# Kernel tuning notes

Measured on AMD Instinct MI355X. Metric: run time of the kernel, lower is better.

Reference implementation:

```python
import jax, jax.numpy as jnp
import numpy as np

D_MODEL = 1024
N_HEADS = 16
HEAD_DIM = D_MODEL // N_HEADS


def setup_inputs() -> dict:
    key = jax.random.key(0)
    k1, k2, k3 = jax.random.split(key, 3)
    x = jax.random.normal(k1, (8, 1024, D_MODEL), dtype=jnp.float32)
    qkv_w = jax.random.normal(k2, (3 * D_MODEL, D_MODEL), dtype=jnp.float32) * 0.02
    qkv_b = jnp.zeros((3 * D_MODEL,), dtype=jnp.float32)
    proj_w = jax.random.normal(k3, (D_MODEL, D_MODEL), dtype=jnp.float32) * 0.02
    proj_b = jnp.zeros((D_MODEL,), dtype=jnp.float32)
    return {"x": x, "qkv_w": qkv_w, "qkv_b": qkv_b, "proj_w": proj_w, "proj_b": proj_b}


def reference(x, qkv_w, qkv_b, proj_w, proj_b):
    B, N, C = x.shape
    H, Dh = N_HEADS, HEAD_DIM
    # fused QKV projection (torch Linear: x @ W^T + b)
    qkv = x @ qkv_w.T + qkv_b                      # [B, N, 3C]
    qkv = qkv.reshape(B, N, 3, H, Dh).transpose(2, 0, 3, 1, 4)  # [3, B, H, N, Dh]
    q, k, v = qkv[0], qkv[1], qkv[2]
    scale = Dh ** -0.5
    attn = jnp.einsum("bhnd,bhmd->bhnm", q, k) * scale  # [B, H, N, N]
    attn = jax.nn.softmax(attn, axis=-1)
    out = jnp.einsum("bhnm,bhmd->bhnd", attn, v)        # [B, H, N, Dh]
    out = out.transpose(0, 2, 1, 3).reshape(B, N, C)
    return out @ proj_w.T + proj_b
```

## Files before the change

kernel.cpp:

```cpp
#include <hip/hip_runtime.h>
#include <hip/hip_bf16.h>
#include <stdint.h>

#define D_MODEL 1024
#define NHEADS  16
#define HDIM    64
#define SEQ     1024
#define BATCH   8

typedef __bf16 bf16;
typedef bf16  bf16x8 __attribute__((ext_vector_type(8)));
typedef float f32x4  __attribute__((ext_vector_type(4)));
typedef uint32_t u32;

__device__ __forceinline__ int swzi(int row, int col) {
    return (row << 6) + (col ^ ((row & 7) << 3));
}

__device__ __forceinline__ void gload_lds16(const bf16* g, bf16* l) {
    __builtin_amdgcn_global_load_lds(
        (const __attribute__((address_space(1))) void*)g,
        (__attribute__((address_space(3))) void*)l, 16, 0, 0);
}

__global__ void cvt_kernel(const float* __restrict__ in, bf16* __restrict__ out, int n) {
    int i = (blockIdx.x * 256 + threadIdx.x) * 8;
    if (i >= n) return;
    float4 a = *reinterpret_cast<const float4*>(in + i);
    float4 b = *reinterpret_cast<const float4*>(in + i + 4);
    union { bf16 h[8]; uint4 u; } pk;
    pk.h[0] = (bf16)a.x; pk.h[1] = (bf16)a.y; pk.h[2] = (bf16)a.z; pk.h[3] = (bf16)a.w;
    pk.h[4] = (bf16)b.x; pk.h[5] = (bf16)b.y; pk.h[6] = (bf16)b.z; pk.h[7] = (bf16)b.w;
    *reinterpret_cast<uint4*>(out + i) = pk.u;
}

__device__ __forceinline__ void gemm_tile_acc(
    const bf16* __restrict__ A, const bf16* __restrict__ B, int K,
    int m0, int n0, bf16* As, bf16* Bs,
    f32x4 acc[4][4], int wr, int wc, int lane, int tid)
{
    for (int kt = 0; kt < K; kt += 64) {
        __syncthreads();
#pragma unroll
        for (int c = 0; c < 4; ++c) {
            int chunk = tid + c * 256;
            int r   = chunk >> 3;
            int j   = chunk & 7;
            int jg  = j ^ (r & 7);
            gload_lds16(A + (size_t)(m0 + r) * K + kt + jg * 8, As + chunk * 8);
            gload_lds16(B + (size_t)(n0 + r) * K + kt + jg * 8, Bs + chunk * 8);
        }
        __syncthreads();
#pragma unroll
        for (int kk = 0; kk < 2; ++kk) {
            bf16x8 af[4], bfr[4];
#pragma unroll
            for (int t = 0; t < 4; ++t) {
                af[t]  = *reinterpret_cast<const bf16x8*>(As + swzi(wr * 64 + t * 16 + (lane & 15), kk * 32 + ((lane >> 4) << 3)));
                bfr[t] = *reinterpret_cast<const bf16x8*>(Bs + swzi(wc * 64 + t * 16 + (lane & 15), kk * 32 + ((lane >> 4) << 3)));
            }
#pragma unroll
            for (int i = 0; i < 4; ++i)
#pragma unroll
                for (int j2 = 0; j2 < 4; ++j2)
                    acc[i][j2] = __builtin_amdgcn_mfma_f32_16x16x32_bf16(af[i], bfr[j2], acc[i][j2], 0, 0, 0);
        }
    }
}

__global__ __launch_bounds__(256)
void qkv_gemm(const bf16* __restrict__ X, const bf16* __restrict__ W,
              const float* __restrict__ bias,
              bf16* __restrict__ q_ws, bf16* __restrict__ k_ws, bf16* __restrict__ vt_ws)
{
    __shared__ __align__(16) bf16 As[128 * 64];
    __shared__ __align__(16) bf16 Bs[128 * 64];
    const int NB = 3072 / 128;
    int bm = blockIdx.x / NB, bn = blockIdx.x % NB;
    int m0 = bm * 128, n0 = bn * 128;
    int tid = threadIdx.x, lane = tid & 63, w = tid >> 6;
    int wr = w >> 1, wc = w & 1;
    f32x4 acc[4][4];
#pragma unroll
    for (int i = 0; i < 4; ++i)
#pragma unroll
        for (int j = 0; j < 4; ++j) acc[i][j] = (f32x4){0.f, 0.f, 0.f, 0.f};

    gemm_tile_acc(X, W, 1024, m0, n0, As, Bs, acc, wr, wc, lane, tid);

#pragma unroll
    for (int i = 0; i < 4; ++i) {
        int mbase = m0 + wr * 64 + i * 16 + ((lane >> 4) << 2);
#pragma unroll
        for (int j = 0; j < 4; ++j) {
            int col = n0 + wc * 64 + j * 16 + (lane & 15);
            int which = col >> 10, rem = col & 1023;
            int h = rem >> 6, d = rem & 63;
            float bi = bias[col];
            int b = mbase >> 10, nrow0 = mbase & 1023;
            int bh = b * NHEADS + h;
            if (which == 2) {
                union { bf16 h4[4]; uint2 u; } vp;
#pragma unroll
                for (int r = 0; r < 4; ++r) vp.h4[r] = (bf16)(acc[i][j][r] + bi);
                *reinterpret_cast<uint2*>(vt_ws + ((size_t)bh * HDIM + d) * SEQ + nrow0) = vp.u;
            } else {
                bf16* dst = (which == 0) ? q_ws : k_ws;
                float scl = (which == 0) ? 0.125f : 1.0f;
#pragma unroll
                for (int r = 0; r < 4; ++r) {
                    float v = (acc[i][j][r] + bi) * scl;
                    dst[((size_t)bh * SEQ + nrow0 + r) * HDIM + d] = (bf16)v;
                }
            }
        }
    }
}

__global__ __launch_bounds__(256)
void proj_gemm(const bf16* __restrict__ Ao, const bf16* __restrict__ W,
               const float* __restrict__ bias, float* __restrict__ out)
{
    __shared__ __align__(16) bf16 As[128 * 64];
    __shared__ __align__(16) bf16 Bs[128 * 64];
    const int NB = 1024 / 128;
    int bm = blockIdx.x / NB, bn = blockIdx.x % NB;
    int m0 = bm * 128, n0 = bn * 128;
    int tid = threadIdx.x, lane = tid & 63, w = tid >> 6;
    int wr = w >> 1, wc = w & 1;
    f32x4 acc[4][4];
#pragma unroll
    for (int i = 0; i < 4; ++i)
#pragma unroll
        for (int j = 0; j < 4; ++j) acc[i][j] = (f32x4){0.f, 0.f, 0.f, 0.f};

    gemm_tile_acc(Ao, W, 1024, m0, n0, As, Bs, acc, wr, wc, lane, tid);

#pragma unroll
    for (int i = 0; i < 4; ++i) {
        int mbase = m0 + wr * 64 + i * 16 + ((lane >> 4) << 2);
#pragma unroll
        for (int j = 0; j < 4; ++j) {
            int col = n0 + wc * 64 + j * 16 + (lane & 15);
            float bi = bias[col];
#pragma unroll
            for (int r = 0; r < 4; ++r)
                out[(size_t)(mbase + r) * D_MODEL + col] = acc[i][j][r] + bi;
        }
    }
}

__global__ __launch_bounds__(256)
void attn_kernel(const bf16* __restrict__ Q, const bf16* __restrict__ K,
                 const bf16* __restrict__ Vt, bf16* __restrict__ AO)
{
    __shared__ __align__(16) bf16 kl[64 * 64];
    __shared__ __align__(16) bf16 vl[64 * 64];
    int bh = blockIdx.x & 127;
    int qt = blockIdx.x >> 7;
    int tid = threadIdx.x, lane = tid & 63, w = tid >> 6;
    int g = lane >> 4, q = lane & 15;
    const bf16* Qb  = Q  + (size_t)bh * SEQ * HDIM;
    const bf16* Kb  = K  + (size_t)bh * SEQ * HDIM;
    const bf16* Vtb = Vt + (size_t)bh * HDIM * SEQ;

    int qrow = qt * 64 + w * 16 + q;
    bf16x8 qf[2];
#pragma unroll
    for (int kk = 0; kk < 2; ++kk)
        qf[kk] = *reinterpret_cast<const bf16x8*>(Qb + (size_t)qrow * HDIM + kk * 32 + (g << 3));

    f32x4 o[4];
#pragma unroll
    for (int dt = 0; dt < 4; ++dt) o[dt] = (f32x4){0.f, 0.f, 0.f, 0.f};
    float mrun = -1e30f, lrun = 0.f;

    int srcA = ((g & 1) << 5) + q;
    int srcB = srcA + 16;
    bool hi = (g >> 1) != 0;

    for (int t = 0; t < 16; ++t) {
        __syncthreads();
#pragma unroll
        for (int c = 0; c < 2; ++c) {
            int chunk = tid + c * 256;
            int r  = chunk >> 3;
            int j  = chunk & 7;
            int jg = j ^ (r & 7);
            gload_lds16(Kb  + (size_t)(t * 64 + r) * HDIM + jg * 8, kl + chunk * 8);
            gload_lds16(Vtb + (size_t)r * SEQ + t * 64 + jg * 8,    vl + chunk * 8);
        }
        __syncthreads();

        f32x4 s[4];
#pragma unroll
        for (int nt = 0; nt < 4; ++nt) {
            s[nt] = (f32x4){0.f, 0.f, 0.f, 0.f};
#pragma unroll
            for (int kk = 0; kk < 2; ++kk) {
                bf16x8 kf = *reinterpret_cast<const bf16x8*>(
                    kl + swzi(nt * 16 + q, kk * 32 + (g << 3)));
                s[nt] = __builtin_amdgcn_mfma_f32_16x16x32_bf16(kf, qf[kk], s[nt], 0, 0, 0);
            }
        }

        float pm = s[0][0];
#pragma unroll
        for (int nt = 0; nt < 4; ++nt)
#pragma unroll
            for (int r = 0; r < 4; ++r) pm = fmaxf(pm, s[nt][r]);
        pm = fmaxf(pm, __shfl_xor(pm, 16));
        pm = fmaxf(pm, __shfl_xor(pm, 32));
        float mnew  = fmaxf(mrun, pm);
        float alpha = __expf(mrun - mnew);

        u32 pk[4][2];
        float psum = 0.f;
#pragma unroll
        for (int nt = 0; nt < 4; ++nt)
#pragma unroll
            for (int half = 0; half < 2; ++half) {
                float pa = __expf(s[nt][2 * half]     - mnew);
                float pb = __expf(s[nt][2 * half + 1] - mnew);
                psum += pa + pb;
                union { bf16 h[2]; u32 u; } pw;
                pw.h[0] = (bf16)pa; pw.h[1] = (bf16)pb;
                pk[nt][half] = pw.u;
            }
        psum += __shfl_xor(psum, 16);
        psum += __shfl_xor(psum, 32);
        lrun = lrun * alpha + psum;
        mrun = mnew;
#pragma unroll
        for (int dt = 0; dt < 4; ++dt) o[dt] *= alpha;

#pragma unroll
        for (int ks = 0; ks < 2; ++ks) {
            union { u32 u[4]; bf16x8 v; } pb;
            u32 a0 = __shfl((int)pk[2 * ks][0],     srcA);
            u32 a1 = __shfl((int)pk[2 * ks + 1][0], srcA);
            pb.u[0] = hi ? a1 : a0;
            u32 b0 = __shfl((int)pk[2 * ks][1],     srcA);
            u32 b1 = __shfl((int)pk[2 * ks + 1][1], srcA);
            pb.u[1] = hi ? b1 : b0;
            u32 c0 = __shfl((int)pk[2 * ks][0],     srcB);
            u32 c1 = __shfl((int)pk[2 * ks + 1][0], srcB);
            pb.u[2] = hi ? c1 : c0;
            u32 d0 = __shfl((int)pk[2 * ks][1],     srcB);
            u32 d1 = __shfl((int)pk[2 * ks + 1][1], srcB);
            pb.u[3] = hi ? d1 : d0;
#pragma unroll
            for (int dt = 0; dt < 4; ++dt) {
                bf16x8 vfr = *reinterpret_cast<const bf16x8*>(
                    vl + swzi(dt * 16 + q, ks * 32 + (g << 3)));
                o[dt] = __builtin_amdgcn_mfma_f32_16x16x32_bf16(vfr, pb.v, o[dt], 0, 0, 0);
            }
        }
    }

    int b = bh >> 4, h = bh & 15;
    float inv = 1.f / lrun;
    size_t base = ((size_t)b * SEQ + qrow) * D_MODEL + h * HDIM;
#pragma unroll
    for (int dt = 0; dt < 4; ++dt) {
        union { bf16 h4[4]; uint2 u; } ob;
#pragma unroll
        for (int r = 0; r < 4; ++r) ob.h4[r] = (bf16)(o[dt][r] * inv);
        *reinterpret_cast<uint2*>(AO + base + dt * 16 + (g << 2)) = ob.u;
    }
}

extern "C" void kernel_launch(void* const* d_in, const int* in_sizes, int n_in,
                              void* d_out, int out_size, void* d_ws, size_t ws_size,
                              hipStream_t stream) {
    const float* x      = (const float*)d_in[0];
    const float* qkv_w  = (const float*)d_in[1];
    const float* qkv_b  = (const float*)d_in[2];
    const float* proj_w = (const float*)d_in[3];
    const float* proj_b = (const float*)d_in[4];
    float* out = (float*)d_out;
    char* ws = (char*)d_ws;

    bf16* x_bf    = (bf16*)(ws);
    bf16* wqkv_bf = (bf16*)(ws + (size_t)(16 << 20));
    bf16* wproj_bf= (bf16*)(ws + (size_t)(22 << 20));
    bf16* q_ws    = (bf16*)(ws + (size_t)(24 << 20));
    bf16* k_ws    = (bf16*)(ws + (size_t)(40 << 20));
    bf16* vt_ws   = (bf16*)(ws + (size_t)(56 << 20));
    bf16* ao_ws   = x_bf;

    cvt_kernel<<<(8192 * 1024) / 2048, 256, 0, stream>>>(x, x_bf, 8192 * 1024);
    cvt_kernel<<<(3072 * 1024) / 2048, 256, 0, stream>>>(qkv_w, wqkv_bf, 3072 * 1024);
    cvt_kernel<<<(1024 * 1024) / 2048, 256, 0, stream>>>(proj_w, wproj_bf, 1024 * 1024);

    qkv_gemm<<<64 * 24, 256, 0, stream>>>(x_bf, wqkv_bf, qkv_b, q_ws, k_ws, vt_ws);
    attn_kernel<<<128 * 16, 256, 0, stream>>>(q_ws, k_ws, vt_ws, ao_ws);
    proj_gemm<<<64 * 8, 256, 0, stream>>>(ao_ws, wproj_bf, proj_b, out);
}
```

Before: 188.6 us.

## Process two query tiles per warp in attention, reusing K/V fragments, with exp2 lazy rescaling

Each attention block now covers 128 query rows instead of 64, with each warp handling two 16-row query groups. K and V fragments are loaded from LDS once per tile and reused for both groups, which halves the K/V global and LDS traffic per query. The softmax scale now folds in log2(e) so exp2f can replace expf. A lazy rescale skips the max update while the new max stays within 6 of the running one. The grid is halved, which cuts occupancy and wave count, and the larger fragment arrays raise register pressure.

```diff
diff --git a/kernel.cpp b/kernel.cpp
--- a/kernel.cpp
+++ b/kernel.cpp
@@ -106,7 +106,7 @@
                 *reinterpret_cast<uint2*>(vt_ws + ((size_t)bh * HDIM + d) * SEQ + nrow0) = vp.u;
             } else {
                 bf16* dst = (which == 0) ? q_ws : k_ws;
-                float scl = (which == 0) ? 0.125f : 1.0f;
+                float scl = (which == 0) ? 0.18033688011112042f : 1.0f;
 #pragma unroll
                 for (int r = 0; r < 4; ++r) {
                     float v = (acc[i][j][r] + bi) * scl;
@@ -164,109 +164,148 @@
     const bf16* Kb  = K  + (size_t)bh * SEQ * HDIM;
     const bf16* Vtb = Vt + (size_t)bh * HDIM * SEQ;
 
-    int qrow = qt * 64 + w * 16 + q;
-    bf16x8 qf[2];
-#pragma unroll
-    for (int kk = 0; kk < 2; ++kk)
-        qf[kk] = *reinterpret_cast<const bf16x8*>(Qb + (size_t)qrow * HDIM + kk * 32 + (g << 3));
-
-    f32x4 o[4];
-#pragma unroll
-    for (int dt = 0; dt < 4; ++dt) o[dt] = (f32x4){0.f, 0.f, 0.f, 0.f};
-    float mrun = -1e30f, lrun = 0.f;
+    int qrow0 = qt * 128 + w * 32;
+    bf16x8 qf[2][2];
+#pragma unroll
+    for (int qh = 0; qh < 2; ++qh)
+#pragma unroll
+        for (int kk = 0; kk < 2; ++kk)
+            qf[qh][kk] = *reinterpret_cast<const bf16x8*>(
+                Qb + (size_t)(qrow0 + qh * 16 + q) * HDIM + kk * 32 + (g << 3));
+
+    f32x4 o[2][4];
+#pragma unroll
+    for (int qh = 0; qh < 2; ++qh)
+#pragma unroll
+        for (int dt = 0; dt < 4; ++dt) o[qh][dt] = (f32x4){0.f, 0.f, 0.f, 0.f};
+    float mrun[2] = {-1e30f, -1e30f}, lrun[2] = {0.f, 0.f};
 
     int srcA = ((g & 1) << 5) + q;
     int srcB = srcA + 16;
     bool hi = (g >> 1) != 0;
 
+    const bf16* ksrc[2]; const bf16* vsrc[2]; bf16* kdst[2]; bf16* vdst[2];
+#pragma unroll
+    for (int c = 0; c < 2; ++c) {
+        int chunk = tid + c * 256;
+        int r  = chunk >> 3;
+        int j  = chunk & 7;
+        int jg = j ^ (r & 7);
+        ksrc[c] = Kb  + (size_t)r * HDIM + jg * 8;
+        vsrc[c] = Vtb + (size_t)r * SEQ + jg * 8;
+        kdst[c] = kl + chunk * 8;
+        vdst[c] = vl + chunk * 8;
+    }
+
     for (int t = 0; t < 16; ++t) {
         __syncthreads();
 #pragma unroll
         for (int c = 0; c < 2; ++c) {
-            int chunk = tid + c * 256;
-            int r  = chunk >> 3;
-            int j  = chunk & 7;
-            int jg = j ^ (r & 7);
-            gload_lds16(Kb  + (size_t)(t * 64 + r) * HDIM + jg * 8, kl + chunk * 8);
-            gload_lds16(Vtb + (size_t)r * SEQ + t * 64 + jg * 8,    vl + chunk * 8);
+            gload_lds16(ksrc[c], kdst[c]);
+            gload_lds16(vsrc[c], vdst[c]);
+            ksrc[c] += 64 * HDIM;
+            vsrc[c] += 64;
         }
         __syncthreads();
 
-        f32x4 s[4];
-#pragma unroll
-        for (int nt = 0; nt < 4; ++nt) {
-            s[nt] = (f32x4){0.f, 0.f, 0.f, 0.f};
-#pragma unroll
-            for (int kk = 0; kk < 2; ++kk) {
-                bf16x8 kf = *reinterpret_cast<const bf16x8*>(
+        bf16x8 kf[4][2];
+#pragma unroll
+        for (int nt = 0; nt < 4; ++nt)
+#pragma unroll
+            for (int kk = 0; kk < 2; ++kk)
+                kf[nt][kk] = *reinterpret_cast<const bf16x8*>(
                     kl + swzi(nt * 16 + q, kk * 32 + (g << 3)));
-                s[nt] = __builtin_amdgcn_mfma_f32_16x16x32_bf16(kf, qf[kk], s[nt], 0, 0, 0);
-            }
-        }
-
-        float pm = s[0][0];
-#pragma unroll
-        for (int nt = 0; nt < 4; ++nt)
-#pragma unroll
-            for (int r = 0; r < 4; ++r) pm = fmaxf(pm, s[nt][r]);
-        pm = fmaxf(pm, __shfl_xor(pm, 16));
-        pm = fmaxf(pm, __shfl_xor(pm, 32));
-        float mnew  = fmaxf(mrun, pm);
-        float alpha = __expf(mrun - mnew);
-
-        u32 pk[4][2];
-        float psum = 0.f;
-#pragma unroll
-        for (int nt = 0; nt < 4; ++nt)
-#pragma unroll
-            for (int half = 0; half < 2; ++half) {
-                float pa = __expf(s[nt][2 * half]     - mnew);
-                float pb = __expf(s[nt][2 * half + 1] - mnew);
-                psum += pa + pb;
-                union { bf16 h[2]; u32 u; } pw;
-                pw.h[0] = (bf16)pa; pw.h[1] = (bf16)pb;
-                pk[nt][half] = pw.u;
-            }
-        psum += __shfl_xor(psum, 16);
-        psum += __shfl_xor(psum, 32);
-        lrun = lrun * alpha + psum;
-        mrun = mnew;
-#pragma unroll
-        for (int dt = 0; dt < 4; ++dt) o[dt] *= alpha;
-
-#pragma unroll
-        for (int ks = 0; ks < 2; ++ks) {
-            union { u32 u[4]; bf16x8 v; } pb;
-            u32 a0 = __shfl((int)pk[2 * ks][0],     srcA);
-            u32 a1 = __shfl((int)pk[2 * ks + 1][0], srcA);
-            pb.u[0] = hi ? a1 : a0;
-            u32 b0 = __shfl((int)pk[2 * ks][1],     srcA);
-            u32 b1 = __shfl((int)pk[2 * ks + 1][1], srcA);
-            pb.u[1] = hi ? b1 : b0;
-            u32 c0 = __shfl((int)pk[2 * ks][0],     srcB);
-            u32 c1 = __shfl((int)pk[2 * ks + 1][0], srcB);
-            pb.u[2] = hi ? c1 : c0;
-            u32 d0 = __shfl((int)pk[2 * ks][1],     srcB);
-            u32 d1 = __shfl((int)pk[2 * ks + 1][1], srcB);
-            pb.u[3] = hi ? d1 : d0;
-#pragma unroll
-            for (int dt = 0; dt < 4; ++dt) {
-                bf16x8 vfr = *reinterpret_cast<const bf16x8*>(
+
+        u32 pkk[2][4][2];
+#pragma unroll
+        for (int qh = 0; qh < 2; ++qh) {
+            f32x4 s[4];
+#pragma unroll
+            for (int nt = 0; nt < 4; ++nt) {
+                s[nt] = (f32x4){0.f, 0.f, 0.f, 0.f};
+#pragma unroll
+                for (int kk = 0; kk < 2; ++kk)
+                    s[nt] = __builtin_amdgcn_mfma_f32_16x16x32_bf16(kf[nt][kk], qf[qh][kk], s[nt], 0, 0, 0);
+            }
+
+            float pm = fmaxf(fmaxf(s[0][0], s[0][1]), fmaxf(s[0][2], s[0][3]));
+            pm = fmaxf(fmaxf(pm, s[1][0]), fmaxf(s[1][1], s[1][2]));
+            pm = fmaxf(fmaxf(pm, s[1][3]), fmaxf(s[2][0], s[2][1]));
+            pm = fmaxf(fmaxf(pm, s[2][2]), fmaxf(s[2][3], s[3][0]));
+            pm = fmaxf(fmaxf(pm, s[3][1]), fmaxf(s[3][2], s[3][3]));
+            pm = fmaxf(pm, __shfl_xor(pm, 16));
+            pm = fmaxf(pm, __shfl_xor(pm, 32));
+
+            if (!__all(pm - mrun[qh] <= 6.f)) {
+                float mnew  = fmaxf(mrun[qh], pm);
+                float alpha = exp2f(mrun[qh] - mnew);
+                lrun[qh] *= alpha;
+                mrun[qh] = mnew;
+#pragma unroll
+                for (int dt = 0; dt < 4; ++dt) o[qh][dt] *= alpha;
+            }
+
+            float m2 = mrun[qh];
+            float psum = 0.f;
+#pragma unroll
+            for (int nt = 0; nt < 4; ++nt)
+#pragma unroll
+                for (int half = 0; half < 2; ++half) {
+                    float pa = exp2f(s[nt][2 * half]     - m2);
+                    float pb = exp2f(s[nt][2 * half + 1] - m2);
+                    psum += pa + pb;
+                    union { bf16 h[2]; u32 u; } pw;
+                    pw.h[0] = (bf16)pa; pw.h[1] = (bf16)pb;
+                    pkk[qh][nt][half] = pw.u;
+                }
+            psum += __shfl_xor(psum, 16);
+            psum += __shfl_xor(psum, 32);
+            lrun[qh] += psum;
+        }
+
+        bf16x8 vfr[4][2];
+#pragma unroll
+        for (int dt = 0; dt < 4; ++dt)
+#pragma unroll
+            for (int ks = 0; ks < 2; ++ks)
+                vfr[dt][ks] = *reinterpret_cast<const bf16x8*>(
                     vl + swzi(dt * 16 + q, ks * 32 + (g << 3)));
-                o[dt] = __builtin_amdgcn_mfma_f32_16x16x32_bf16(vfr, pb.v, o[dt], 0, 0, 0);
-            }
-        }
+
+#pragma unroll
+        for (int qh = 0; qh < 2; ++qh)
+#pragma unroll
+            for (int ks = 0; ks < 2; ++ks) {
+                union { u32 u[4]; bf16x8 v; } pb;
+                u32 a0 = __shfl((int)pkk[qh][2 * ks][0],     srcA);
+                u32 a1 = __shfl((int)pkk[qh][2 * ks + 1][0], srcA);
+                pb.u[0] = hi ? a1 : a0;
+                u32 b0 = __shfl((int)pkk[qh][2 * ks][1],     srcA);
+                u32 b1 = __shfl((int)pkk[qh][2 * ks + 1][1], srcA);
+                pb.u[1] = hi ? b1 : b0;
+                u32 c0 = __shfl((int)pkk[qh][2 * ks][0],     srcB);
+                u32 c1 = __shfl((int)pkk[qh][2 * ks + 1][0], srcB);
+                pb.u[2] = hi ? c1 : c0;
+                u32 d0 = __shfl((int)pkk[qh][2 * ks][1],     srcB);
+                u32 d1 = __shfl((int)pkk[qh][2 * ks + 1][1], srcB);
+                pb.u[3] = hi ? d1 : d0;
+#pragma unroll
+                for (int dt = 0; dt < 4; ++dt)
+                    o[qh][dt] = __builtin_amdgcn_mfma_f32_16x16x32_bf16(vfr[dt][ks], pb.v, o[qh][dt], 0, 0, 0);
+            }
     }
 
     int b = bh >> 4, h = bh & 15;
-    float inv = 1.f / lrun;
-    size_t base = ((size_t)b * SEQ + qrow) * D_MODEL + h * HDIM;
-#pragma unroll
-    for (int dt = 0; dt < 4; ++dt) {
-        union { bf16 h4[4]; uint2 u; } ob;
-#pragma unroll
-        for (int r = 0; r < 4; ++r) ob.h4[r] = (bf16)(o[dt][r] * inv);
-        *reinterpret_cast<uint2*>(AO + base + dt * 16 + (g << 2)) = ob.u;
+#pragma unroll
+    for (int qh = 0; qh < 2; ++qh) {
+        float inv = 1.f / lrun[qh];
+        size_t base = ((size_t)b * SEQ + qrow0 + qh * 16 + q) * D_MODEL + h * HDIM;
+#pragma unroll
+        for (int dt = 0; dt < 4; ++dt) {
+            union { bf16 h4[4]; uint2 u; } ob;
+#pragma unroll
+            for (int r = 0; r < 4; ++r) ob.h4[r] = (bf16)(o[qh][dt][r] * inv);
+            *reinterpret_cast<uint2*>(AO + base + dt * 16 + (g << 2)) = ob.u;
+        }
     }
 }
 
@@ -294,6 +333,6 @@
     cvt_kernel<<<(1024 * 1024) / 2048, 256, 0, stream>>>(proj_w, wproj_bf, 1024 * 1024);
 
     qkv_gemm<<<64 * 24, 256, 0, stream>>>(x_bf, wqkv_bf, qkv_b, q_ws, k_ws, vt_ws);
-    attn_kernel<<<128 * 16, 256, 0, stream>>>(q_ws, k_ws, vt_ws, ao_ws);
+    attn_kernel<<<128 * 8, 256, 0, stream>>>(q_ws, k_ws, vt_ws, ao_ws);
     proj_gemm<<<64 * 8, 256, 0, stream>>>(ao_ws, wproj_bf, proj_b, out);
 }
```

Measured after the change: 201.6 us. 6.9% more time.

## Use exp2 softmax with lazy rescaling, hoisted load addresses, and MFMA priority hints

Applied to the files above, without the earlier changes.

Folds log2(e) into the Q scale so the softmax can use exp2 directly. Rescaling of the output accumulator is skipped unless the running max grows by more than a threshold anywhere in the wave. Global-to-LDS source and destination pointers are precomputed once and advanced each iteration, and s_setprio is raised around the MFMA blocks. The lazy rescale leaves exponentials bounded by 2^6 in fp32/bf16 accumulation, which trades a small numerical risk for fewer multiplies per tile.

```diff
diff --git a/kernel.cpp b/kernel.cpp
--- a/kernel.cpp
+++ b/kernel.cpp
@@ -106,7 +106,7 @@
                 *reinterpret_cast<uint2*>(vt_ws + ((size_t)bh * HDIM + d) * SEQ + nrow0) = vp.u;
             } else {
                 bf16* dst = (which == 0) ? q_ws : k_ws;
-                float scl = (which == 0) ? 0.125f : 1.0f;
+                float scl = (which == 0) ? 0.18033688011112042f : 1.0f;
 #pragma unroll
                 for (int r = 0; r < 4; ++r) {
                     float v = (acc[i][j][r] + bi) * scl;
@@ -179,20 +179,32 @@
     int srcB = srcA + 16;
     bool hi = (g >> 1) != 0;
 
+    const bf16* ksrc[2]; const bf16* vsrc[2]; bf16* kdst[2]; bf16* vdst[2];
+#pragma unroll
+    for (int c = 0; c < 2; ++c) {
+        int chunk = tid + c * 256;
+        int r  = chunk >> 3;
+        int j  = chunk & 7;
+        int jg = j ^ (r & 7);
+        ksrc[c] = Kb  + (size_t)r * HDIM + jg * 8;
+        vsrc[c] = Vtb + (size_t)r * SEQ + jg * 8;
+        kdst[c] = kl + chunk * 8;
+        vdst[c] = vl + chunk * 8;
+    }
+
     for (int t = 0; t < 16; ++t) {
         __syncthreads();
 #pragma unroll
         for (int c = 0; c < 2; ++c) {
-            int chunk = tid + c * 256;
-            int r  = chunk >> 3;
-            int j  = chunk & 7;
-            int jg = j ^ (r & 7);
-            gload_lds16(Kb  + (size_t)(t * 64 + r) * HDIM + jg * 8, kl + chunk * 8);
-            gload_lds16(Vtb + (size_t)r * SEQ + t * 64 + jg * 8,    vl + chunk * 8);
+            gload_lds16(ksrc[c], kdst[c]);
+            gload_lds16(vsrc[c], vdst[c]);
+            ksrc[c] += 64 * HDIM;
+            vsrc[c] += 64;
         }
         __syncthreads();
 
         f32x4 s[4];
+        __builtin_amdgcn_s_setprio(1);
 #pragma unroll
         for (int nt = 0; nt < 4; ++nt) {
             s[nt] = (f32x4){0.f, 0.f, 0.f, 0.f};
@@ -203,58 +215,66 @@
                 s[nt] = __builtin_amdgcn_mfma_f32_16x16x32_bf16(kf, qf[kk], s[nt], 0, 0, 0);
             }
         }
-
-        float pm = s[0][0];
-#pragma unroll
-        for (int nt = 0; nt < 4; ++nt)
-#pragma unroll
-            for (int r = 0; r < 4; ++r) pm = fmaxf(pm, s[nt][r]);
+        __builtin_amdgcn_s_setprio(0);
+
+        float pm = fmaxf(fmaxf(s[0][0], s[0][1]), fmaxf(s[0][2], s[0][3]));
+        pm = fmaxf(fmaxf(pm, s[1][0]), fmaxf(s[1][1], s[1][2]));
+        pm = fmaxf(fmaxf(pm, s[1][3]), fmaxf(s[2][0], s[2][1]));
+        pm = fmaxf(fmaxf(pm, s[2][2]), fmaxf(s[2][3], s[3][0]));
+        pm = fmaxf(fmaxf(pm, s[3][1]), fmaxf(s[3][2], s[3][3]));
         pm = fmaxf(pm, __shfl_xor(pm, 16));
         pm = fmaxf(pm, __shfl_xor(pm, 32));
-        float mnew  = fmaxf(mrun, pm);
-        float alpha = __expf(mrun - mnew);
-
-        u32 pk[4][2];
+
+        if (!__all(pm - mrun <= 6.f)) {
+            float mnew  = fmaxf(mrun, pm);
+            float alpha = exp2f(mrun - mnew);
+            lrun *= alpha;
+            mrun = mnew;
+#pragma unroll
+            for (int dt = 0; dt < 4; ++dt) o[dt] *= alpha;
+        }
+
+        float m2 = mrun;
+        u32 pkk[4][2];
         float psum = 0.f;
 #pragma unroll
         for (int nt = 0; nt < 4; ++nt)
 #pragma unroll
             for (int half = 0; half < 2; ++half) {
-                float pa = __expf(s[nt][2 * half]     - mnew);
-                float pb = __expf(s[nt][2 * half + 1] - mnew);
+                float pa = exp2f(s[nt][2 * half]     - m2);
+                float pb = exp2f(s[nt][2 * half + 1] - m2);
                 psum += pa + pb;
                 union { bf16 h[2]; u32 u; } pw;
                 pw.h[0] = (bf16)pa; pw.h[1] = (bf16)pb;
-                pk[nt][half] = pw.u;
+                pkk[nt][half] = pw.u;
             }
         psum += __shfl_xor(psum, 16);
         psum += __shfl_xor(psum, 32);
-        lrun = lrun * alpha + psum;
-        mrun = mnew;
-#pragma unroll
-        for (int dt = 0; dt < 4; ++dt) o[dt] *= alpha;
+        lrun += psum;
 
 #pragma unroll
         for (int ks = 0; ks < 2; ++ks) {
             union { u32 u[4]; bf16x8 v; } pb;
-            u32 a0 = __shfl((int)pk[2 * ks][0],     srcA);
-            u32 a1 = __shfl((int)pk[2 * ks + 1][0], srcA);
+            u32 a0 = __shfl((int)pkk[2 * ks][0],     srcA);
+            u32 a1 = __shfl((int)pkk[2 * ks + 1][0], srcA);
             pb.u[0] = hi ? a1 : a0;
-            u32 b0 = __shfl((int)pk[2 * ks][1],     srcA);
-            u32 b1 = __shfl((int)pk[2 * ks + 1][1], srcA);
+            u32 b0 = __shfl((int)pkk[2 * ks][1],     srcA);
+            u32 b1 = __shfl((int)pkk[2 * ks + 1][1], srcA);
             pb.u[1] = hi ? b1 : b0;
-            u32 c0 = __shfl((int)pk[2 * ks][0],     srcB);
-            u32 c1 = __shfl((int)pk[2 * ks + 1][0], srcB);
+            u32 c0 = __shfl((int)pkk[2 * ks][0],     srcB);
+            u32 c1 = __shfl((int)pkk[2 * ks + 1][0], srcB);
             pb.u[2] = hi ? c1 : c0;
-            u32 d0 = __shfl((int)pk[2 * ks][1],     srcB);
-            u32 d1 = __shfl((int)pk[2 * ks + 1][1], srcB);
+            u32 d0 = __shfl((int)pkk[2 * ks][1],     srcB);
+            u32 d1 = __shfl((int)pkk[2 * ks + 1][1], srcB);
             pb.u[3] = hi ? d1 : d0;
+            __builtin_amdgcn_s_setprio(1);
 #pragma unroll
             for (int dt = 0; dt < 4; ++dt) {
                 bf16x8 vfr = *reinterpret_cast<const bf16x8*>(
                     vl + swzi(dt * 16 + q, ks * 32 + (g << 3)));
                 o[dt] = __builtin_amdgcn_mfma_f32_16x16x32_bf16(vfr, pb.v, o[dt], 0, 0, 0);
             }
+            __builtin_amdgcn_s_setprio(0);
         }
     }
 
```

Result: slower. 196.1 us (+4.0%).
